# Optimization experiments

Hardware: AMD Instinct MI355X
Metric: run time of the kernel (lower is better)

## Reference

```python
import jax, jax.numpy as jnp
import numpy as np

K, PMAX, NUM_PTS = 20000, 30, 5
GEO_DIM, PE_DIM = 256, 32
C_OUT = GEO_DIM - PE_DIM  # 224
NUM_FREQS = 8


def setup_inputs() -> dict:
    key = jax.random.key(0)
    k = jax.random.split(key, 6)
    geoms = jax.random.normal(k[0], (K, PMAX, 2), dtype=jnp.float32) * 8.0  # ego BEV meters
    lengths = jax.random.randint(k[1], (K,), 2, PMAX + 1)                   # valid points per polyline
    w1 = jax.random.normal(k[2], (C_OUT // 2, 2, 3), jnp.float32) * 0.2
    b1 = jax.random.normal(k[3], (C_OUT // 2,), jnp.float32) * 0.02
    w2 = jax.random.normal(k[4], (C_OUT, C_OUT // 2, 3), jnp.float32) * 0.05
    b2 = jax.random.normal(k[5], (C_OUT,), jnp.float32) * 0.02
    gamma = jnp.ones((C_OUT,), jnp.float32)
    beta = jnp.zeros((C_OUT,), jnp.float32)
    return {"geoms": geoms, "lengths": lengths, "w1": w1, "b1": b1,
            "w2": w2, "b2": b2, "gamma": gamma, "beta": beta,
            "roi_w": 60, "roi_h": 30}


def _resample_one(coords, L):
    # coords: [PMAX,2] padded polyline; L: scalar int (>=2 valid points)
    diffs = coords[1:] - coords[:-1]                                  # [PMAX-1,2]
    sq = jnp.sum(diffs * diffs, axis=1)
    mask = (jnp.arange(PMAX - 1) < (L - 1)).astype(coords.dtype)      # valid segments
    seg = jnp.where(sq > 0, jnp.sqrt(jnp.where(sq > 0, sq, 1.0)), 0.0) * mask
    cum = jnp.concatenate([jnp.zeros((1,), coords.dtype), jnp.cumsum(seg)])  # [PMAX]
    total = cum[-1]
    targets = jnp.linspace(0.0, 1.0, NUM_PTS, dtype=coords.dtype) * total
    idx = jnp.clip(jnp.searchsorted(cum, targets, side='left'), 1, L - 1)
    t = (targets - cum[idx - 1]) / (seg[idx - 1] + 1e-8)
    pts = coords[idx - 1] + t[:, None] * diffs[idx - 1]               # [NUM_PTS,2]
    degen = total < 1e-6
    return jnp.where(degen, jnp.broadcast_to(coords[0], pts.shape), pts)


def _conv1d(x, w, b):
    # x: [K,C,5]; w: [O,C,3]; 'same' padding 1
    y = jax.lax.conv_general_dilated(x, w, (1,), ((1, 1),),
                                     dimension_numbers=('NCH', 'OIH', 'NCH'))
    return y + b[None, :, None]


def reference(geoms, lengths, w1, b1, w2, b2, gamma, beta, roi_w, roi_h):
    resampled = jax.vmap(_resample_one)(geoms, lengths)               # [K,5,2]
    roi_half = jnp.array([roi_w / 2.0, roi_h / 2.0], jnp.float32)
    roi_full = jnp.array([float(roi_w), float(roi_h)], jnp.float32)
    coords = (resampled + roi_half) / roi_full                        # [K,5,2] in [0,1]
    # sinusoidal PE: per coord dim [sin(x*2^f*pi) x8 | cos x8] -> flatten to 32
    freqs = (2.0 ** jnp.arange(NUM_FREQS, dtype=jnp.float32)) * np.float32(np.pi)
    xf = coords[..., None] * freqs                                    # [K,5,2,8]
    pe = jnp.concatenate([jnp.sin(xf), jnp.cos(xf)], axis=-1).reshape(-1, NUM_PTS, PE_DIM)
    x = coords.transpose(0, 2, 1)                                     # [K,2,5]
    x = jax.nn.relu(_conv1d(x, w1, b1))                               # [K,112,5]
    x = jax.nn.relu(_conv1d(x, w2, b2))                               # [K,224,5]
    x = x.transpose(0, 2, 1)                                          # [K,5,224]
    mu = jnp.mean(x, axis=-1, keepdims=True)
    var = jnp.mean((x - mu) ** 2, axis=-1, keepdims=True)
    x = (x - mu) * jax.lax.rsqrt(var + 1e-5) * gamma + beta
    geo_feats = jnp.concatenate([pe, x], axis=-1)                     # [K,5,256]
    return geo_feats, coords
```

## Files before the change

### kernel.cpp

```cpp
#include <hip/hip_runtime.h>
#include <math.h>

#define K_POLY   20000
#define PMAX     30
#define NUM_PTS  5
#define C_MID    112
#define C_OUT    224
#define PE_DIM   32
#define GEO_DIM  256
#define M_ROWS   (K_POLY*NUM_PTS)

#define NTILES   14
#define KSTEPS   11
#define WP_ELEMS (KSTEPS*NTILES*64*8)
#define NPACK_BLK ((WP_ELEMS+255)/256)
#define POLY_PER_BLK 4
#define NPREP_BLK ((K_POLY+POLY_PER_BLK-1)/POLY_PER_BLK)

#define CHUNK_STRIDE 2560
#define CHUNK_OFF    64

#define ROWS_W   30
#define WAVES_B  4
#define NWAVES2  ((M_ROWS+ROWS_W-1)/ROWS_W)
#define NBLK2    ((NWAVES2+WAVES_B-1)/WAVES_B)

typedef __attribute__((ext_vector_type(8))) short short8;
typedef __attribute__((ext_vector_type(4))) float f32x4;

__device__ inline unsigned short f2bf(float f) {
    union { float f; unsigned u; } v; v.f = f;
    return (unsigned short)((v.u + 0x7fffu + ((v.u >> 16) & 1u)) >> 16);
}

#define GLDS(gp, lp) __builtin_amdgcn_global_load_lds( \
    (const __attribute__((address_space(1))) void*)(gp), \
    (__attribute__((address_space(3))) void*)(lp), 16, 0, 0)

__global__ __launch_bounds__(256) void prep_pack(
    const float* __restrict__ geoms, const int* __restrict__ lengths,
    const float* __restrict__ w1, const float* __restrict__ b1,
    const float* __restrict__ w2,
    const int* __restrict__ roi_w, const int* __restrict__ roi_h,
    unsigned short* __restrict__ Wp, float* __restrict__ out)
{
    if (blockIdx.x < NPACK_BLK) {
        int i = blockIdx.x * 256 + threadIdx.x;
        if (i < WP_ELEMS) {
            int j    = i & 7;
            int lane = (i >> 3) & 63;
            int grp  = i >> 9;
            int nt   = grp % NTILES;
            int ks   = grp / NTILES;
            int k    = ks * 32 + (lane >> 4) * 8 + j;
            int n    = nt * 16 + (lane & 15);
            float v = 0.f;
            if (k < 336) {
                int dk = k / C_MID, c = k - dk * C_MID;
                v = w2[(n * C_MID + c) * 3 + dk];
            }
            Wp[i] = f2bf(v);
        }
        return;
    }

    const int poly = (blockIdx.x - NPACK_BLK) * POLY_PER_BLK + (threadIdx.x >> 6);
    const int lane = threadIdx.x & 63;
    if (poly >= K_POLY) return;

    const float* gp = geoms + (size_t)poly * (PMAX * 2);
    float px = 0.f, py = 0.f;
    if (lane < PMAX) { float2 p = ((const float2*)gp)[lane]; px = p.x; py = p.y; }
    const int L = lengths[poly];

    float nx = __shfl(px, lane + 1);
    float ny = __shfl(py, lane + 1);
    float seg = 0.f;
    if (lane < L - 1 && lane < PMAX - 1) {
        float dx = nx - px, dy = ny - py;
        float sq = dx * dx + dy * dy;
        seg = (sq > 0.f) ? sqrtf(sq) : 0.f;
    }
    float incl = seg;
    #pragma unroll
    for (int d = 1; d < 32; d <<= 1) {
        float v = __shfl_up(incl, d, 32);
        if ((lane & 31) >= d) incl += v;
    }
    float cum = __shfl_up(incl, 1, 32);
    if ((lane & 31) == 0) cum = 0.f;
    const float total = __shfl(incl, PMAX - 2);

    const float roiw = (float)roi_w[0], roih = (float)roi_h[0];
    const float halfx = roiw * 0.5f, halfy = roih * 0.5f;
    const bool degen = total < 1e-6f;
    const float x0g = __shfl(px, 0), y0g = __shfl(py, 0);

    float bxv[NUM_PTS], byv[NUM_PTS];
    #pragma unroll
    for (int j = 0; j < NUM_PTS; ++j) {
        float tj = total * (0.25f * (float)j);
        unsigned long long mlt = __ballot(lane < PMAX && cum < tj);
        int idx = (int)__popcll(mlt);
        idx = max(1, min(idx, L - 1));
        float c1 = __shfl(cum, idx - 1);
        float s1 = __shfl(seg, idx - 1);
        float ax = __shfl(px, idx - 1), ay = __shfl(py, idx - 1);
        float bx2 = __shfl(px, idx),    by2 = __shfl(py, idx);
        float tt = (tj - c1) / (s1 + 1e-8f);
        float fx = degen ? x0g : ax + tt * (bx2 - ax);
        float fy = degen ? y0g : ay + tt * (by2 - ay);
        bxv[j] = (fx + halfx) / roiw;
        byv[j] = (fy + halfy) / roih;
    }
    if (lane == 0) {
        float* co = out + (size_t)M_ROWS * GEO_DIM + (size_t)poly * (NUM_PTS * 2);
        #pragma unroll
        for (int j = 0; j < NUM_PTS; ++j) { co[2 * j] = bxv[j]; co[2 * j + 1] = byv[j]; }
    }

    unsigned short* chunk = (unsigned short*)out + (size_t)poly * CHUNK_STRIDE + CHUNK_OFF;
    unsigned int* cz = (unsigned int*)chunk;
    if (lane < 56) cz[lane] = 0u;
    cz[336 + lane] = 0u;

    #pragma unroll
    for (int it = 0; it < 2; ++it) {
        int c = it * 64 + lane;
        if (c < C_MID) {
            const float* w = w1 + c * 6;
            float w0 = w[0], wa = w[1], wb = w[2], w3 = w[3], w4 = w[4], w5 = w[5];
            float bb = b1[c];
            #pragma unroll
            for (int p = 0; p < NUM_PTS; ++p) {
                float acc = bb + bxv[p] * wa + byv[p] * w4;
                if (p > 0)           acc += bxv[p - 1] * w0 + byv[p - 1] * w3;
                if (p < NUM_PTS - 1) acc += bxv[p + 1] * wb + byv[p + 1] * w5;
                chunk[(p + 1) * C_MID + c] = f2bf(fmaxf(acc, 0.f));
            }
        }
    }
}

__global__ __launch_bounds__(256, 3) void gemm2(
    const unsigned short* __restrict__ Wp,
    const float* __restrict__ b2, const float* __restrict__ gamma,
    const float* __restrict__ beta, float* __restrict__ out)
{
    __shared__ __align__(16) unsigned short s_B[2][NTILES * 512];

    const int t = threadIdx.x, lane = t & 63, wave = t >> 6;
    const int quad = lane >> 4, m = lane & 15;
    const int rw = (blockIdx.x * WAVES_B + wave) * ROWS_W;

    int r0 = min(rw + m, M_ROWS - 1);
    int r1 = min(rw + 16 + m, M_ROWS - 1);
    int poly0 = r0 / 5, p0 = r0 - poly0 * 5;
    int poly1 = r1 / 5, p1 = r1 - poly1 * 5;
    const unsigned short* A = (const unsigned short*)out;
    const unsigned short* Ab0 = A + (size_t)poly0 * CHUNK_STRIDE + CHUNK_OFF + p0 * C_MID + quad * 8;
    const unsigned short* Ab1 = A + (size_t)poly1 * CHUNK_STRIDE + CHUNK_OFF + p1 * C_MID + quad * 8;

    f32x4 acc0[NTILES], acc1[NTILES];
    #pragma unroll
    for (int nt = 0; nt < NTILES; ++nt)
        #pragma unroll
        for (int i = 0; i < 4; ++i) { acc0[nt][i] = 0.f; acc1[nt][i] = 0.f; }

    const char* WpB = (const char*)Wp;
    #pragma unroll
    for (int j = 0; j < 4; ++j) {
        int sgi = j * WAVES_B + wave;
        if (sgi < NTILES)
            GLDS(WpB + sgi * 1024 + lane * 16, (char*)&s_B[0][0] + sgi * 1024);
    }
    short8 a0 = *(const short8*)Ab0;
    short8 a1 = *(const short8*)Ab1;
    __syncthreads();

    int buf = 0;
    for (int ks = 0; ks < KSTEPS; ++ks) {
        short8 a0n = a0, a1n = a1;
        if (ks < KSTEPS - 1) {
            const char* src = WpB + (size_t)(ks + 1) * (NTILES * 1024);
            #pragma unroll
            for (int j = 0; j < 4; ++j) {
                int sgi = j * WAVES_B + wave;
                if (sgi < NTILES)
                    GLDS(src + sgi * 1024 + lane * 16, (char*)&s_B[buf ^ 1][0] + sgi * 1024);
            }
            a0n = *(const short8*)(Ab0 + (ks + 1) * 32);
            a1n = *(const short8*)(Ab1 + (ks + 1) * 32);
        }
        const unsigned short* bp = &s_B[buf][lane * 8];
        #pragma unroll
        for (int nt = 0; nt < NTILES; ++nt) {
            short8 b = *(const short8*)(bp + nt * 512);
            acc0[nt] = __builtin_amdgcn_mfma_f32_16x16x32_bf16(a0, b, acc0[nt], 0, 0, 0);
            acc1[nt] = __builtin_amdgcn_mfma_f32_16x16x32_bf16(a1, b, acc1[nt], 0, 0, 0);
        }
        __syncthreads();
        buf ^= 1; a0 = a0n; a1 = a1n;
    }

    {
        const float* cptr = out + (size_t)M_ROWS * GEO_DIM;
        const int col = lane & 31;
        const int d = col >> 4, isc = (col >> 3) & 1, fr = col & 7;
        const float pef = (float)(1 << fr) * 3.14159265358979323846f;
        #pragma unroll
        for (int it = 0; it < 15; ++it) {
            int r = rw + it * 2 + (lane >> 5);
            if (r < M_ROWS) {
                float x = cptr[(size_t)r * 2 + d];
                float arg = x * pef;
                out[(size_t)r * GEO_DIM + col] = isc ? __cosf(arg) : __sinf(arg);
            }
        }
    }

    float bias[NTILES], gm[NTILES], bt[NTILES];
    #pragma unroll
    for (int nt = 0; nt < NTILES; ++nt) {
        int col = nt * 16 + m;
        bias[nt] = b2[col]; gm[nt] = gamma[col]; bt[nt] = beta[col];
    }

    auto epilogue = [&](f32x4 (&acc)[NTILES], int g) {
        #pragma unroll
        for (int i = 0; i < 4; ++i) {
            float s = 0.f, q = 0.f;
            #pragma unroll
            for (int nt = 0; nt < NTILES; ++nt) {
                float v = fmaxf(acc[nt][i] + bias[nt], 0.f);
                acc[nt][i] = v;
                s += v; q += v * v;
            }
            #pragma unroll
            for (int mk = 8; mk >= 1; mk >>= 1) {
                s += __shfl_xor(s, mk, 64);
                q += __shfl_xor(q, mk, 64);
            }
            float mu  = s * (1.f / C_OUT);
            float var = fmaxf(q * (1.f / C_OUT) - mu * mu, 0.f);
            float rs  = rsqrtf(var + 1e-5f);
            int r = rw + g * 16 + quad * 4 + i;
            if (r < M_ROWS && !(g == 1 && quad == 3 && i >= 2)) {
                size_t ob = (size_t)r * GEO_DIM + PE_DIM + m;
                #pragma unroll
                for (int nt = 0; nt < NTILES; ++nt)
                    out[ob + nt * 16] = (acc[nt][i] - mu) * rs * gm[nt] + bt[nt];
            }
        }
    };
    epilogue(acc0, 0);
    epilogue(acc1, 1);
}

extern "C" void kernel_launch(void* const* d_in, const int* in_sizes, int n_in,
                              void* d_out, int out_size, void* d_ws, size_t ws_size,
                              hipStream_t stream) {
    const float* geoms   = (const float*)d_in[0];
    const int*   lengths = (const int*)d_in[1];
    const float* w1      = (const float*)d_in[2];
    const float* b1      = (const float*)d_in[3];
    const float* w2      = (const float*)d_in[4];
    const float* b2      = (const float*)d_in[5];
    const float* gamma   = (const float*)d_in[6];
    const float* beta    = (const float*)d_in[7];
    const int*   roi_w   = (const int*)d_in[8];
    const int*   roi_h   = (const int*)d_in[9];
    float* out = (float*)d_out;
    unsigned short* Wp = (unsigned short*)d_ws;

    hipLaunchKernelGGL(prep_pack, dim3(NPACK_BLK + NPREP_BLK), dim3(256), 0, stream,
                       geoms, lengths, w1, b1, w2, roi_w, roi_h, Wp, out);
    hipLaunchKernelGGL(gemm2, dim3(NBLK2), dim3(256), 0, stream, Wp, b2, gamma, beta, out);
}
```

Measured before the change: 194.3 us.

## Load GEMM B fragments directly from global instead of LDS double buffering

Removes the LDS double-buffered staging of the packed weight matrix (global_load_lds plus per-step barriers). Each wave now reads its B fragments straight from global memory (L1/L2-resident, shared across waves), fully unrolls the K loop and raises wave priority around the MFMA block. Occupancy hint drops from 3 to 2 blocks per CU to give the larger unrolled register footprint room. This trades barrier and LDS traffic for redundant per-wave global/cache reads and higher register pressure.

```diff
diff --git a/kernel.cpp b/kernel.cpp
--- a/kernel.cpp
+++ b/kernel.cpp
@@ -32,10 +32,6 @@
     union { float f; unsigned u; } v; v.f = f;
     return (unsigned short)((v.u + 0x7fffu + ((v.u >> 16) & 1u)) >> 16);
 }
-
-#define GLDS(gp, lp) __builtin_amdgcn_global_load_lds( \
-    (const __attribute__((address_space(1))) void*)(gp), \
-    (__attribute__((address_space(3))) void*)(lp), 16, 0, 0)
 
 __global__ __launch_bounds__(256) void prep_pack(
     const float* __restrict__ geoms, const int* __restrict__ lengths,
@@ -142,13 +138,11 @@
     }
 }
 
-__global__ __launch_bounds__(256, 3) void gemm2(
+__global__ __launch_bounds__(256, 2) void gemm2(
     const unsigned short* __restrict__ Wp,
     const float* __restrict__ b2, const float* __restrict__ gamma,
     const float* __restrict__ beta, float* __restrict__ out)
 {
-    __shared__ __align__(16) unsigned short s_B[2][NTILES * 512];
-
     const int t = threadIdx.x, lane = t & 63, wave = t >> 6;
     const int quad = lane >> 4, m = lane & 15;
     const int rw = (blockIdx.x * WAVES_B + wave) * ROWS_W;
@@ -161,46 +155,28 @@
     const unsigned short* Ab0 = A + (size_t)poly0 * CHUNK_STRIDE + CHUNK_OFF + p0 * C_MID + quad * 8;
     const unsigned short* Ab1 = A + (size_t)poly1 * CHUNK_STRIDE + CHUNK_OFF + p1 * C_MID + quad * 8;
 
+    const short8* Bl = (const short8*)(Wp + lane * 8);
+
     f32x4 acc0[NTILES], acc1[NTILES];
     #pragma unroll
     for (int nt = 0; nt < NTILES; ++nt)
         #pragma unroll
         for (int i = 0; i < 4; ++i) { acc0[nt][i] = 0.f; acc1[nt][i] = 0.f; }
 
-    const char* WpB = (const char*)Wp;
-    #pragma unroll
-    for (int j = 0; j < 4; ++j) {
-        int sgi = j * WAVES_B + wave;
-        if (sgi < NTILES)
-            GLDS(WpB + sgi * 1024 + lane * 16, (char*)&s_B[0][0] + sgi * 1024);
-    }
-    short8 a0 = *(const short8*)Ab0;
-    short8 a1 = *(const short8*)Ab1;
-    __syncthreads();
-
-    int buf = 0;
+    #pragma unroll
     for (int ks = 0; ks < KSTEPS; ++ks) {
-        short8 a0n = a0, a1n = a1;
-        if (ks < KSTEPS - 1) {
-            const char* src = WpB + (size_t)(ks + 1) * (NTILES * 1024);
-            #pragma unroll
-            for (int j = 0; j < 4; ++j) {
-                int sgi = j * WAVES_B + wave;
-                if (sgi < NTILES)
-                    GLDS(src + sgi * 1024 + lane * 16, (char*)&s_B[buf ^ 1][0] + sgi * 1024);
-            }
-            a0n = *(const short8*)(Ab0 + (ks + 1) * 32);
-            a1n = *(const short8*)(Ab1 + (ks + 1) * 32);
-        }
-        const unsigned short* bp = &s_B[buf][lane * 8];
+        short8 a0 = *(const short8*)(Ab0 + ks * 32);
+        short8 a1 = *(const short8*)(Ab1 + ks * 32);
+        short8 b[NTILES];
+        #pragma unroll
+        for (int nt = 0; nt < NTILES; ++nt) b[nt] = Bl[(ks * NTILES + nt) * 64];
+        __builtin_amdgcn_s_setprio(1);
         #pragma unroll
         for (int nt = 0; nt < NTILES; ++nt) {
-            short8 b = *(const short8*)(bp + nt * 512);
-            acc0[nt] = __builtin_amdgcn_mfma_f32_16x16x32_bf16(a0, b, acc0[nt], 0, 0, 0);
-            acc1[nt] = __builtin_amdgcn_mfma_f32_16x16x32_bf16(a1, b, acc1[nt], 0, 0, 0);
-        }
-        __syncthreads();
-        buf ^= 1; a0 = a0n; a1 = a1n;
+            acc0[nt] = __builtin_amdgcn_mfma_f32_16x16x32_bf16(a0, b[nt], acc0[nt], 0, 0, 0);
+            acc1[nt] = __builtin_amdgcn_mfma_f32_16x16x32_bf16(a1, b[nt], acc1[nt], 0, 0, 0);
+        }
+        __builtin_amdgcn_s_setprio(0);
     }
 
     {
```

New measurement: 178.1 us. -8.3%, faster.

## Make gemm2 persistent with full weight matrix resident in LDS

Applied to the files above, without the earlier changes.

Instead of streaming each 14-tile weight slice through a double-buffered LDS ring per 30-row wave unit, each block of 8 waves loads the whole packed W2 matrix (about 158 KB bf16) into LDS once and then loops over row units grid-stride with 256 blocks. This removes the per-k-step __syncthreads and the repeated global-to-LDS weight reloads for every block, and adds s_setprio around the MFMA bursts. The cost is a large LDS footprint that limits occupancy to one block per CU, and a single up-front load before any compute.

```diff
diff --git a/kernel.cpp b/kernel.cpp
--- a/kernel.cpp
+++ b/kernel.cpp
@@ -21,9 +21,10 @@
 #define CHUNK_OFF    64
 
 #define ROWS_W   30
-#define WAVES_B  4
-#define NWAVES2  ((M_ROWS+ROWS_W-1)/ROWS_W)
-#define NBLK2    ((NWAVES2+WAVES_B-1)/WAVES_B)
+#define NUNITS   ((M_ROWS+ROWS_W-1)/ROWS_W)
+#define WAVES2_B 8
+#define NBLK2    256
+#define TOTW2    (NBLK2*WAVES2_B)
 
 typedef __attribute__((ext_vector_type(8))) short short8;
 typedef __attribute__((ext_vector_type(4))) float f32x4;
@@ -142,119 +143,117 @@
     }
 }
 
-__global__ __launch_bounds__(256, 3) void gemm2(
+__global__ __launch_bounds__(512, 2) void gemm2(
     const unsigned short* __restrict__ Wp,
     const float* __restrict__ b2, const float* __restrict__ gamma,
     const float* __restrict__ beta, float* __restrict__ out)
 {
-    __shared__ __align__(16) unsigned short s_B[2][NTILES * 512];
+    __shared__ __align__(16) unsigned short s_B[WP_ELEMS];
 
     const int t = threadIdx.x, lane = t & 63, wave = t >> 6;
     const int quad = lane >> 4, m = lane & 15;
-    const int rw = (blockIdx.x * WAVES_B + wave) * ROWS_W;
-
-    int r0 = min(rw + m, M_ROWS - 1);
-    int r1 = min(rw + 16 + m, M_ROWS - 1);
-    int poly0 = r0 / 5, p0 = r0 - poly0 * 5;
-    int poly1 = r1 / 5, p1 = r1 - poly1 * 5;
+
+    #pragma unroll
+    for (int it = 0; it < 20; ++it) {
+        int idx = t + it * 512;
+        if (idx < WP_ELEMS / 8)
+            GLDS((const char*)Wp + (size_t)idx * 16, (char*)s_B + idx * 16);
+    }
+    __syncthreads();
+
     const unsigned short* A = (const unsigned short*)out;
-    const unsigned short* Ab0 = A + (size_t)poly0 * CHUNK_STRIDE + CHUNK_OFF + p0 * C_MID + quad * 8;
-    const unsigned short* Ab1 = A + (size_t)poly1 * CHUNK_STRIDE + CHUNK_OFF + p1 * C_MID + quad * 8;
-
-    f32x4 acc0[NTILES], acc1[NTILES];
-    #pragma unroll
-    for (int nt = 0; nt < NTILES; ++nt)
-        #pragma unroll
-        for (int i = 0; i < 4; ++i) { acc0[nt][i] = 0.f; acc1[nt][i] = 0.f; }
-
-    const char* WpB = (const char*)Wp;
-    #pragma unroll
-    for (int j = 0; j < 4; ++j) {
-        int sgi = j * WAVES_B + wave;
-        if (sgi < NTILES)
-            GLDS(WpB + sgi * 1024 + lane * 16, (char*)&s_B[0][0] + sgi * 1024);
-    }
-    short8 a0 = *(const short8*)Ab0;
-    short8 a1 = *(const short8*)Ab1;
-    __syncthreads();
-
-    int buf = 0;
-    for (int ks = 0; ks < KSTEPS; ++ks) {
-        short8 a0n = a0, a1n = a1;
-        if (ks < KSTEPS - 1) {
-            const char* src = WpB + (size_t)(ks + 1) * (NTILES * 1024);
-            #pragma unroll
-            for (int j = 0; j < 4; ++j) {
-                int sgi = j * WAVES_B + wave;
-                if (sgi < NTILES)
-                    GLDS(src + sgi * 1024 + lane * 16, (char*)&s_B[buf ^ 1][0] + sgi * 1024);
-            }
-            a0n = *(const short8*)(Ab0 + (ks + 1) * 32);
-            a1n = *(const short8*)(Ab1 + (ks + 1) * 32);
-        }
-        const unsigned short* bp = &s_B[buf][lane * 8];
+    const float* cptr = out + (size_t)M_ROWS * GEO_DIM;
+    const unsigned short* bl = s_B + lane * 8;
+
+    for (int u = blockIdx.x * WAVES2_B + wave; u < NUNITS; u += TOTW2) {
+        const int rw = u * ROWS_W;
+
+        int r0 = min(rw + m, M_ROWS - 1);
+        int r1 = min(rw + 16 + m, M_ROWS - 1);
+        int poly0 = r0 / 5, p0 = r0 - poly0 * 5;
+        int poly1 = r1 / 5, p1 = r1 - poly1 * 5;
+        const unsigned short* Ab0 = A + (size_t)poly0 * CHUNK_STRIDE + CHUNK_OFF + p0 * C_MID + quad * 8;
+        const unsigned short* Ab1 = A + (size_t)poly1 * CHUNK_STRIDE + CHUNK_OFF + p1 * C_MID + quad * 8;
+
+        f32x4 acc0[NTILES], acc1[NTILES];
+        #pragma unroll
+        for (int nt = 0; nt < NTILES; ++nt)
+            #pragma unroll
+            for (int i = 0; i < 4; ++i) { acc0[nt][i] = 0.f; acc1[nt][i] = 0.f; }
+
+        short8 a0 = *(const short8*)Ab0;
+        short8 a1 = *(const short8*)Ab1;
+        #pragma unroll
+        for (int ks = 0; ks < KSTEPS; ++ks) {
+            short8 a0n = a0, a1n = a1;
+            if (ks < KSTEPS - 1) {
+                a0n = *(const short8*)(Ab0 + (ks + 1) * 32);
+                a1n = *(const short8*)(Ab1 + (ks + 1) * 32);
+            }
+            const unsigned short* bp = bl + ks * (NTILES * 512);
+            __builtin_amdgcn_s_setprio(1);
+            #pragma unroll
+            for (int nt = 0; nt < NTILES; ++nt) {
+                short8 b = *(const short8*)(bp + nt * 512);
+                acc0[nt] = __builtin_amdgcn_mfma_f32_16x16x32_bf16(a0, b, acc0[nt], 0, 0, 0);
+                acc1[nt] = __builtin_amdgcn_mfma_f32_16x16x32_bf16(a1, b, acc1[nt], 0, 0, 0);
+            }
+            __builtin_amdgcn_s_setprio(0);
+            a0 = a0n; a1 = a1n;
+        }
+
+        {
+            const int col = lane & 31;
+            const int d = col >> 4, isc = (col >> 3) & 1, fr = col & 7;
+            const float pef = (float)(1 << fr) * 3.14159265358979323846f;
+            #pragma unroll
+            for (int it = 0; it < 15; ++it) {
+                int r = rw + it * 2 + (lane >> 5);
+                if (r < M_ROWS) {
+                    float x = cptr[(size_t)r * 2 + d];
+                    float arg = x * pef;
+                    out[(size_t)r * GEO_DIM + col] = isc ? __cosf(arg) : __sinf(arg);
+                }
+            }
+        }
+
+        float bias[NTILES], gm[NTILES], bt[NTILES];
         #pragma unroll
         for (int nt = 0; nt < NTILES; ++nt) {
-            short8 b = *(const short8*)(bp + nt * 512);
-            acc0[nt] = __builtin_amdgcn_mfma_f32_16x16x32_bf16(a0, b, acc0[nt], 0, 0, 0);
-            acc1[nt] = __builtin_amdgcn_mfma_f32_16x16x32_bf16(a1, b, acc1[nt], 0, 0, 0);
-        }
-        __syncthreads();
-        buf ^= 1; a0 = a0n; a1 = a1n;
-    }
-
-    {
-        const float* cptr = out + (size_t)M_ROWS * GEO_DIM;
-        const int col = lane & 31;
-        const int d = col >> 4, isc = (col >> 3) & 1, fr = col & 7;
-        const float pef = (float)(1 << fr) * 3.14159265358979323846f;
-        #pragma unroll
-        for (int it = 0; it < 15; ++it) {
-            int r = rw + it * 2 + (lane >> 5);
-            if (r < M_ROWS) {
-                float x = cptr[(size_t)r * 2 + d];
-                float arg = x * pef;
-                out[(size_t)r * GEO_DIM + col] = isc ? __cosf(arg) : __sinf(arg);
-            }
-        }
-    }
-
-    float bias[NTILES], gm[NTILES], bt[NTILES];
-    #pragma unroll
-    for (int nt = 0; nt < NTILES; ++nt) {
-        int col = nt * 16 + m;
-        bias[nt] = b2[col]; gm[nt] = gamma[col]; bt[nt] = beta[col];
-    }
-
-    auto epilogue = [&](f32x4 (&acc)[NTILES], int g) {
-        #pragma unroll
-        for (int i = 0; i < 4; ++i) {
-            float s = 0.f, q = 0.f;
-            #pragma unroll
-            for (int nt = 0; nt < NTILES; ++nt) {
-                float v = fmaxf(acc[nt][i] + bias[nt], 0.f);
-                acc[nt][i] = v;
-                s += v; q += v * v;
-            }
-            #pragma unroll
-            for (int mk = 8; mk >= 1; mk >>= 1) {
-                s += __shfl_xor(s, mk, 64);
-                q += __shfl_xor(q, mk, 64);
-            }
-            float mu  = s * (1.f / C_OUT);
-            float var = fmaxf(q * (1.f / C_OUT) - mu * mu, 0.f);
-            float rs  = rsqrtf(var + 1e-5f);
-            int r = rw + g * 16 + quad * 4 + i;
-            if (r < M_ROWS && !(g == 1 && quad == 3 && i >= 2)) {
-                size_t ob = (size_t)r * GEO_DIM + PE_DIM + m;
+            int col = nt * 16 + m;
+            bias[nt] = b2[col]; gm[nt] = gamma[col]; bt[nt] = beta[col];
+        }
+
+        #pragma unroll
+        for (int g = 0; g < 2; ++g) {
+            f32x4* acc = g ? acc1 : acc0;
+            #pragma unroll
+            for (int i = 0; i < 4; ++i) {
+                float s = 0.f, q = 0.f;
                 #pragma unroll
-                for (int nt = 0; nt < NTILES; ++nt)
-                    out[ob + nt * 16] = (acc[nt][i] - mu) * rs * gm[nt] + bt[nt];
-            }
-        }
-    };
-    epilogue(acc0, 0);
-    epilogue(acc1, 1);
+                for (int nt = 0; nt < NTILES; ++nt) {
+                    float v = fmaxf(acc[nt][i] + bias[nt], 0.f);
+                    acc[nt][i] = v;
+                    s += v; q += v * v;
+                }
+                #pragma unroll
+                for (int mk = 8; mk >= 1; mk >>= 1) {
+                    s += __shfl_xor(s, mk, 64);
+                    q += __shfl_xor(q, mk, 64);
+                }
+                float mu  = s * (1.f / C_OUT);
+                float var = fmaxf(q * (1.f / C_OUT) - mu * mu, 0.f);
+                float rs  = rsqrtf(var + 1e-5f);
+                int r = rw + g * 16 + quad * 4 + i;
+                if (r < M_ROWS && !(g == 1 && quad == 3 && i >= 2)) {
+                    size_t ob = (size_t)r * GEO_DIM + PE_DIM + m;
+                    #pragma unroll
+                    for (int nt = 0; nt < NTILES; ++nt)
+                        out[ob + nt * 16] = (acc[nt][i] - mu) * rs * gm[nt] + bt[nt];
+                }
+            }
+        }
+    }
 }
 
 extern "C" void kernel_launch(void* const* d_in, const int* in_sizes, int n_in,
@@ -275,5 +274,5 @@
 
     hipLaunchKernelGGL(prep_pack, dim3(NPACK_BLK + NPREP_BLK), dim3(256), 0, stream,
                        geoms, lengths, w1, b1, w2, roi_w, roi_h, Wp, out);
-    hipLaunchKernelGGL(gemm2, dim3(NBLK2), dim3(256), 0, stream, Wp, b2, gamma, beta, out);
-}
+    hipLaunchKernelGGL(gemm2, dim3(NBLK2), dim3(512), 0, stream, Wp, b2, gamma, beta, out);
+}
```

After: 166.3 us. 14.4% less time.
